# Kernel optimization log

Hardware: AMD Instinct MI355X
Metric: run time of the kernel (lower is better)

The kernel has to match this reference:

```python
import jax, jax.numpy as jnp
import numpy as np
from jax import lax

D_MODEL = 1024
D_INNER = 2048
B = 8
T = 2048
INIT_ALPHA_BIAS = 2.0


def setup_inputs() -> dict:
    key = jax.random.key(0)
    ks = jax.random.split(key, 6)
    def xavier(k, shape):
        fan_in, fan_out = shape[1], shape[0]
        lim = float(np.sqrt(6.0 / (fan_in + fan_out)))
        return jax.random.uniform(k, shape, jnp.float32, -lim, lim)
    return {
        "x": jax.random.normal(ks[0], (B, T, D_MODEL), jnp.float32),
        "h0": jnp.zeros((B, D_INNER), jnp.float32),
        "W_in": xavier(ks[1], (D_INNER, D_MODEL)),
        "W_alpha": xavier(ks[2], (D_INNER, D_INNER)),
        "b_alpha": jnp.full((D_INNER,), INIT_ALPHA_BIAS, jnp.float32),
        "W_v": xavier(ks[3], (D_INNER, D_INNER)),
        "b_v": jnp.zeros((D_INNER,), jnp.float32),
        "W_out": xavier(ks[4], (D_MODEL, D_INNER)),
    }


def reference(x, h0, W_in, W_alpha, b_alpha, W_v, b_v, W_out):
    # in_proj + silu pre-activation: [B,T,D_inner]
    x_proj = jax.nn.silu(jnp.einsum('btd,id->bti', x, W_in))
    # time-major for the scan: [T,B,D_inner]
    xr = jnp.transpose(x_proj, (1, 0, 2))
    # precompute gate and value for all steps (big GEMMs)
    alpha = jax.nn.sigmoid(jnp.einsum('tbd,ed->tbe', xr, W_alpha) + b_alpha)
    v = jnp.einsum('tbd,ed->tbe', xr, W_v) + b_v

    def step(h, av):
        a, vt = av
        h_new = a * h + (1.0 - a) * vt  # decay-gated update
        out_t = h_new * jax.nn.silu(h_new)  # self-gating
        return h_new, out_t

    h_final, outs = lax.scan(step, h0, (alpha, v))  # outs: [T,B,D_inner]
    # out_proj back to model dim, batch-major: [B,T,D_model]
    output = jnp.einsum('tbe,de->btd', outs, W_out)
    return output, h_final
```

## Files before the change

kernel.cpp:

```cpp
#include <hip/hip_runtime.h>
#include <cstdint>
#include <cstddef>

typedef unsigned short u16;
typedef unsigned int   u32;

#define D_MODEL 1024
#define D_INNER 2048
#define BATCH   8
#define TSEQ    2048
#define MROWS   (BATCH*TSEQ)
#define CHUNK   32
#define NCHUNK  (TSEQ/CHUNK)
#define EDIM    (BATCH*D_INNER)

typedef float  f32x4  __attribute__((ext_vector_type(4)));
typedef __bf16 bf16x8 __attribute__((ext_vector_type(8)));
typedef short  s16x8  __attribute__((ext_vector_type(8)));

__device__ __forceinline__ float bf2f(u16 u){ return __builtin_bit_cast(float, (u32)u << 16); }
__device__ __forceinline__ u16 f2bf(float f){
  u32 u = __builtin_bit_cast(u32, f);
  u += 0x7fffu + ((u >> 16) & 1u);
  return (u16)(u >> 16);
}
__device__ __forceinline__ float sigm(float x){ return 1.0f/(1.0f + __expf(-x)); }

__device__ __forceinline__ void gld16(const u16* g, u16* l){
  __builtin_amdgcn_global_load_lds((const __attribute__((address_space(1))) void*)g,
                                   (__attribute__((address_space(3))) void*)l, 16, 0, 0);
}

__device__ __forceinline__ s16x8 cvt8(const float* s){
  float4 u0 = *(const float4*)s;
  float4 u1 = *(const float4*)(s + 4);
  s16x8 p;
  p[0]=(short)f2bf(u0.x); p[1]=(short)f2bf(u0.y);
  p[2]=(short)f2bf(u0.z); p[3]=(short)f2bf(u0.w);
  p[4]=(short)f2bf(u1.x); p[5]=(short)f2bf(u1.y);
  p[6]=(short)f2bf(u1.z); p[7]=(short)f2bf(u1.w);
  return p;
}

#define LOADA(AF, MH) \
  _Pragma("unroll") \
  for (int mf = 0; mf < 4; ++mf){ \
    AF[mf][0] = *(const s16x8*)(As + (wr*128 + (MH)*64 + mf*16 + l15)*128 + csw); \
    AF[mf][1] = *(const s16x8*)(As + (wr*128 + (MH)*64 + mf*16 + l15)*128 + (csw^64)); \
  }
#define LOADB(BF, NH) \
  _Pragma("unroll") \
  for (int nf = 0; nf < 2; ++nf){ \
    BF[nf][0] = *(const s16x8*)(Bs + (wc*64 + (NH)*32 + nf*16 + l15)*128 + csw); \
    BF[nf][1] = *(const s16x8*)(Bs + (wc*64 + (NH)*32 + nf*16 + l15)*128 + (csw^64)); \
  }
#define MFMAQ(AF, BF, MH, NH) \
  __builtin_amdgcn_s_setprio(1); \
  _Pragma("unroll") \
  for (int mf = 0; mf < 4; ++mf) \
    _Pragma("unroll") \
    for (int nf = 0; nf < 2; ++nf) \
      _Pragma("unroll") \
      for (int ks = 0; ks < 2; ++ks) \
        acc[(MH)*4+mf][(NH)*2+nf] = __builtin_amdgcn_mfma_f32_16x16x32_bf16( \
            __builtin_bit_cast(bf16x8, AF[mf][ks]), \
            __builtin_bit_cast(bf16x8, BF[nf][ks]), \
            acc[(MH)*4+mf][(NH)*2+nf], 0, 0, 0); \
  __builtin_amdgcn_s_setprio(0);

template<int MODE, int K, int N>
__global__ __launch_bounds__(512, 2) void gemm256(
    const u16* __restrict__ A, const u16* __restrict__ Bt,
    const float* __restrict__ bias, const float* __restrict__ bias2,
    void* __restrict__ Cout, void* __restrict__ Cout2)
{
  __shared__ __align__(16) u16 sAB[2][2][16384];
  constexpr int NT = K/64;
  const int tid = threadIdx.x;
  const int w = tid >> 6, lane = tid & 63;
  const int wr = w >> 2, wc = w & 3;
  const int l15 = lane & 15, kg = lane >> 4;
  const int bm = blockIdx.x, bn = blockIdx.y;

  const int st_rw   = lane >> 3;
  const int st_cole = ((lane&7) ^ st_rw) << 3;
  const size_t a_base = (size_t)(bm*256)*K + st_cole;
  const size_t b_base = (size_t)(bn*256)*K + st_cole;

  auto stageA = [&](int buf, int kt, int set){
    u16* dst = &sAB[0][buf][set*4096 + w*512];
    #pragma unroll
    for (int i = 0; i < 2; ++i){
      const int row = set*64 + i*128 + w*8 + st_rw;
      gld16(A + a_base + (size_t)row*K + kt*64, dst + i*8192);
    }
  };
  auto stageB = [&](int buf, int kt, int set){
    #pragma unroll
    for (int i = 0; i < 2; ++i){
      const int g = i*64 + w*8;
      const int rowbase = (g>>5)*64 + set*32 + (g&31);
      gld16(Bt + b_base + (size_t)(rowbase + st_rw)*K + kt*64,
            &sAB[1][buf][rowbase*64]);
    }
  };

  const int csw = (kg*16) ^ ((l15&7)<<4);

  f32x4 acc[8][4] = {};

  stageB(0,0,0); stageA(0,0,0); stageB(0,0,1); stageA(0,0,1);
  asm volatile("s_waitcnt vmcnt(4)" ::: "memory");
  __builtin_amdgcn_s_barrier();

  for (int t = 0; t < NT; ++t){
    const char* As = (const char*)&sAB[0][t&1][0];
    const char* Bs = (const char*)&sAB[1][t&1][0];
    const int nb = (t+1)&1;
    const bool more = (t < NT-1);
    s16x8 af[4][2], bf0[2][2], bf1[2][2];

    LOADA(af, 0)
    LOADB(bf0, 0)
    if (more){
      stageB(nb, t+1, 0); stageA(nb, t+1, 0);
      asm volatile("s_waitcnt vmcnt(6)" ::: "memory");
    } else {
      asm volatile("s_waitcnt vmcnt(2)" ::: "memory");
    }
    __builtin_amdgcn_s_barrier();
    MFMAQ(af, bf0, 0, 0)
    __builtin_amdgcn_s_barrier();

    LOADB(bf1, 1)
    if (more){
      stageB(nb, t+1, 1);
      asm volatile("s_waitcnt vmcnt(6)" ::: "memory");
    } else {
      asm volatile("s_waitcnt vmcnt(0)" ::: "memory");
    }
    __builtin_amdgcn_s_barrier();
    MFMAQ(af, bf1, 0, 1)
    __builtin_amdgcn_s_barrier();

    LOADA(af, 1)
    if (more){ stageA(nb, t+1, 1); }
    __builtin_amdgcn_s_barrier();
    MFMAQ(af, bf1, 1, 1)
    __builtin_amdgcn_s_barrier();

    if (more){
      asm volatile("s_waitcnt vmcnt(4)" ::: "memory");
    }
    __builtin_amdgcn_s_barrier();
    MFMAQ(af, bf0, 1, 0)
    __builtin_amdgcn_s_barrier();
  }

  #pragma unroll
  for (int mi = 0; mi < 8; ++mi){
    #pragma unroll
    for (int ni = 0; ni < 4; ++ni){
      #pragma unroll
      for (int r = 0; r < 4; ++r){
        const int row = bm*256 + wr*128 + mi*16 + kg*4 + r;
        const int col = bn*256 + wc*64 + ni*16 + l15;
        float val = acc[mi][ni][r];
        if constexpr (MODE == 0){
          val = val * sigm(val);
          ((u16*)Cout)[(size_t)row*N + col] = f2bf(val);
        } else if constexpr (MODE == 3){
          const int orow = (row & 7)*TSEQ + (row >> 3);
          ((float*)Cout)[(size_t)orow*N + col] = val;
        } else if constexpr (MODE == 4){
          if (col < D_INNER){
            val = sigm(val + bias[col]);
            ((u16*)Cout)[(size_t)row*D_INNER + col] = f2bf(val);
          } else {
            val = val + bias2[col - D_INNER];
            ((u16*)Cout2)[(size_t)row*D_INNER + (col - D_INNER)] = f2bf(val);
          }
        }
      }
    }
  }
}

template<int MODE, int K, int N, bool BA, bool BB>
__global__ __launch_bounds__(256) void gemm_bt(
    const void* __restrict__ Ap, const void* __restrict__ Bp,
    const float* __restrict__ bias, void* __restrict__ Cout)
{
  __shared__ __align__(16) u16 sA[128*32];
  __shared__ __align__(16) u16 sB[128*32];
  const int tid = threadIdx.x;
  const int bm = blockIdx.x, bn = blockIdx.y;
  const int w = tid >> 6, lane = tid & 63;
  const int wr = w >> 1, wc = w & 1;
  const int l15 = lane & 15, kg = lane >> 4;
  const int r0   = tid >> 2;
  const int koff = (tid & 3) * 8;

  int ga[2];
  #pragma unroll
  for (int i = 0; i < 2; ++i){
    int mc = bm*128 + r0 + i*64;
    if (MODE == 0)      ga[i] = (mc & 7) * TSEQ + (mc >> 3);
    else if (MODE == 3) ga[i] = (mc & (TSEQ-1)) * BATCH + (mc >> 11);
    else                ga[i] = mc;
  }
  const u16*   Abf = (const u16*)Ap;
  const float* Af  = (const float*)Ap;
  const u16*   Bbf = (const u16*)Bp;
  const float* Bf  = (const float*)Bp;
  u16* la[2] = { sA + w*512, sA + 2048 + w*512 };
  u16* lb[2] = { sB + w*512, sB + 2048 + w*512 };
  u16* ldsA = sA + tid*8;
  u16* ldsB = sB + tid*8;
  const int gb[2] = { bn*128 + r0, bn*128 + r0 + 64 };

  f32x4 acc[4][4] = {};
  for (int kt = 0; kt < K/32; ++kt){
    __syncthreads();
    if constexpr (BA){
      gld16(Abf + (size_t)ga[0]*K + koff + kt*32, la[0]);
      gld16(Abf + (size_t)ga[1]*K + koff + kt*32, la[1]);
    } else {
      #pragma unroll
      for (int i = 0; i < 2; ++i)
        *(s16x8*)(ldsA + i*2048) = cvt8(Af + (size_t)ga[i]*K + koff + kt*32);
    }
    if constexpr (BB){
      gld16(Bbf + (size_t)gb[0]*K + koff + kt*32, lb[0]);
      gld16(Bbf + (size_t)gb[1]*K + koff + kt*32, lb[1]);
    } else {
      #pragma unroll
      for (int i = 0; i < 2; ++i)
        *(s16x8*)(ldsB + i*2048) = cvt8(Bf + (size_t)gb[i]*K + koff + kt*32);
    }
    __syncthreads();

    s16x8 af[4], bfr[4];
    #pragma unroll
    for (int m = 0; m < 4; ++m)
      af[m] = *(const s16x8*)(sA + (wr*64 + m*16 + l15)*32 + kg*8);
    #pragma unroll
    for (int n = 0; n < 4; ++n)
      bfr[n] = *(const s16x8*)(sB + (wc*64 + n*16 + l15)*32 + kg*8);
    #pragma unroll
    for (int m = 0; m < 4; ++m)
      #pragma unroll
      for (int n = 0; n < 4; ++n)
        acc[m][n] = __builtin_amdgcn_mfma_f32_16x16x32_bf16(
            __builtin_bit_cast(bf16x8, af[m]),
            __builtin_bit_cast(bf16x8, bfr[n]),
            acc[m][n], 0, 0, 0);
  }
  #pragma unroll
  for (int m = 0; m < 4; ++m)
    #pragma unroll
    for (int n = 0; n < 4; ++n)
      #pragma unroll
      for (int r = 0; r < 4; ++r){
        const int row = bm*128 + wr*64 + m*16 + kg*4 + r;
        const int col = bn*128 + wc*64 + n*16 + l15;
        float val = acc[m][n][r];
        if constexpr (MODE == 0){
          val = val * sigm(val);
          ((u16*)Cout)[(size_t)row*N + col] = f2bf(val);
        } else if constexpr (MODE == 1){
          val = sigm(val + bias[col]);
          ((u16*)Cout)[(size_t)row*N + col] = f2bf(val);
        } else if constexpr (MODE == 2){
          val = val + bias[col];
          ((u16*)Cout)[(size_t)row*N + col] = f2bf(val);
        } else {
          ((float*)Cout)[(size_t)row*N + col] = val;
        }
      }
}

__global__ __launch_bounds__(256) void scan_pass1(
    const u16* __restrict__ alpha, const u16* __restrict__ v,
    float* __restrict__ P, float* __restrict__ H)
{
  const int e = blockIdx.x*256 + threadIdx.x;
  const int c = blockIdx.y;
  const size_t base = (size_t)c*CHUNK*EDIM + e;
  float p = 1.f, h = 0.f;
  #pragma unroll 8
  for (int t = 0; t < CHUNK; ++t){
    float a  = bf2f(alpha[base + (size_t)t*EDIM]);
    float vv = bf2f(v[base + (size_t)t*EDIM]);
    p *= a;
    h = a*h + (1.f - a)*vv;
  }
  P[(size_t)c*EDIM + e] = p;
  H[(size_t)c*EDIM + e] = h;
}

__global__ __launch_bounds__(256) void scan_pass2(
    const float* __restrict__ P, const float* __restrict__ H,
    const float* __restrict__ h0, float* __restrict__ hstart,
    float* __restrict__ hfinal)
{
  const int e = blockIdx.x*256 + threadIdx.x;
  float hs = h0[e];
  for (int c = 0; c < NCHUNK; ++c){
    hstart[(size_t)c*EDIM + e] = hs;
    hs = P[(size_t)c*EDIM + e]*hs + H[(size_t)c*EDIM + e];
  }
  hfinal[e] = hs;
}

__global__ __launch_bounds__(256) void scan_pass3(
    const u16* __restrict__ alpha, const u16* __restrict__ v,
    const float* __restrict__ hstart, u16* __restrict__ outs)
{
  const int e = blockIdx.x*256 + threadIdx.x;
  const int c = blockIdx.y;
  const size_t base = (size_t)c*CHUNK*EDIM + e;
  float h = hstart[(size_t)c*EDIM + e];
  #pragma unroll 8
  for (int t = 0; t < CHUNK; ++t){
    float a  = bf2f(alpha[base + (size_t)t*EDIM]);
    float vv = bf2f(v[base + (size_t)t*EDIM]);
    h = a*h + (1.f - a)*vv;
    float o = h*h*sigm(h);
    outs[base + (size_t)t*EDIM] = f2bf(o);
  }
}

__global__ __launch_bounds__(256) void cvt_bf16(
    const float* __restrict__ src, u16* __restrict__ dst, int n4)
{
  const int i = blockIdx.x*256 + threadIdx.x;
  if (i >= n4) return;
  const float4 f = ((const float4*)src)[i];
  u32 w0 = (u32)f2bf(f.x) | ((u32)f2bf(f.y) << 16);
  u32 w1 = (u32)f2bf(f.z) | ((u32)f2bf(f.w) << 16);
  ((uint2*)dst)[i] = make_uint2(w0, w1);
}

__global__ __launch_bounds__(256) void cvt_x_tm(
    const float* __restrict__ src, u16* __restrict__ dst)
{
  const int i = blockIdx.x*256 + threadIdx.x;
  const int d4  = i & 255;
  const int rin = i >> 8;
  const int b = rin >> 11, tt = rin & (TSEQ-1);
  const int rout = tt*BATCH + b;
  const float4 f = ((const float4*)src)[i];
  u32 w0 = (u32)f2bf(f.x) | ((u32)f2bf(f.y) << 16);
  u32 w1 = (u32)f2bf(f.z) | ((u32)f2bf(f.w) << 16);
  ((uint2*)dst)[(size_t)rout*256 + d4] = make_uint2(w0, w1);
}

extern "C" void kernel_launch(void* const* d_in, const int* in_sizes, int n_in,
                              void* d_out, int out_size, void* d_ws, size_t ws_size,
                              hipStream_t stream)
{
  const float* x     = (const float*)d_in[0];
  const float* h0    = (const float*)d_in[1];
  const float* W_in  = (const float*)d_in[2];
  const float* W_al  = (const float*)d_in[3];
  const float* b_al  = (const float*)d_in[4];
  const float* W_v   = (const float*)d_in[5];
  const float* b_v   = (const float*)d_in[6];
  const float* W_out = (const float*)d_in[7];

  float* out  = (float*)d_out;
  float* hfin = out + (size_t)MROWS*D_MODEL;

  const size_t SZ_ACT = (size_t)MROWS*D_INNER*2;
  const size_t SZ_ST  = (size_t)NCHUNK*EDIM*4;
  const size_t SZ_WI  = (size_t)D_INNER*D_MODEL*2;
  const size_t SZ_WA  = (size_t)D_INNER*D_INNER*2;
  const size_t need_min  = 3*SZ_ACT + 3*SZ_ST;
  const size_t need_fast = need_min + 2*SZ_WI + 2*SZ_WA + 8192;

  if (ws_size < need_min) return;

  char* ws = (char*)d_ws;
  auto carve = [&](size_t bytes){
    char* p = ws; ws += (bytes + 255) & ~(size_t)255; return p;
  };
  u16* xp   = (u16*)carve(SZ_ACT);
  u16* alp  = (u16*)carve(SZ_ACT);
  u16* vv   = (u16*)carve(SZ_ACT);
  float* P  = (float*)carve(SZ_ST);
  float* H  = (float*)carve(SZ_ST);
  float* hs = (float*)carve(SZ_ST);

  const dim3 gScan(EDIM/256, NCHUNK);

  auto cvt = [&](const float* s, u16* d, size_t n){
    int n4 = (int)(n/4);
    cvt_bf16<<<(n4+255)/256, 256, 0, stream>>>(s, d, n4);
  };

  if (ws_size >= need_fast){
    u16* wib = (u16*)carve(SZ_WI);
    u16* wab = (u16*)carve(SZ_WA);
    u16* wvb = (u16*)carve(SZ_WA);
    u16* wob = (u16*)carve(SZ_WI);
    u16* xb  = alp;

    cvt_x_tm<<<(MROWS*D_MODEL/4)/256, 256, 0, stream>>>(x, xb);
    cvt(W_in,  wib, (size_t)D_INNER*D_MODEL);
    cvt(W_al,  wab, (size_t)D_INNER*D_INNER);
    cvt(W_v,   wvb, (size_t)D_INNER*D_INNER);
    cvt(W_out, wob, (size_t)D_MODEL*D_INNER);

    gemm256<0, D_MODEL, D_INNER><<<dim3(MROWS/256, D_INNER/256), 512, 0, stream>>>(
        xb, wib, nullptr, nullptr, xp, nullptr);
    gemm256<4, D_INNER, 2*D_INNER><<<dim3(MROWS/256, 2*D_INNER/256), 512, 0, stream>>>(
        xp, wab, b_al, b_v, alp, vv);

    scan_pass1<<<gScan, 256, 0, stream>>>(alp, vv, P, H);
    scan_pass2<<<EDIM/256, 256, 0, stream>>>(P, H, h0, hs, hfin);
    scan_pass3<<<gScan, 256, 0, stream>>>(alp, vv, hs, vv);

    gemm256<3, D_INNER, D_MODEL><<<dim3(MROWS/256, D_MODEL/256), 512, 0, stream>>>(
        vv, wob, nullptr, nullptr, out, nullptr);
  } else {
    const dim3 gBig(MROWS/128, D_INNER/128);
    const dim3 gOut(MROWS/128, D_MODEL/128);
    gemm_bt<0, D_MODEL, D_INNER, false, false><<<gBig, 256, 0, stream>>>(x,  W_in, nullptr, xp);
    gemm_bt<1, D_INNER, D_INNER, true,  false><<<gBig, 256, 0, stream>>>(xp, W_al, b_al,    alp);
    gemm_bt<2, D_INNER, D_INNER, true,  false><<<gBig, 256, 0, stream>>>(xp, W_v,  b_v,     vv);

    scan_pass1<<<gScan, 256, 0, stream>>>(alp, vv, P, H);
    scan_pass2<<<EDIM/256, 256, 0, stream>>>(P, H, h0, hs, hfin);
    scan_pass3<<<gScan, 256, 0, stream>>>(alp, vv, hs, vv);

    gemm_bt<3, D_INNER, D_MODEL, true, false><<<gOut, 256, 0, stream>>>(vv, W_out, nullptr, out);
  }
}
```

Baseline: 538.9 us.

## Simplify GEMM main loop to one barrier per K-tile with full prefetch

Replaces the four-phase interleaved GEMM schedule with a simpler one. Each K-tile now waits for all outstanding global-to-LDS loads and hits a single barrier. It then issues all next-tile loads at once and runs the full 8x4 MFMA block, loading all B fragments up front. This removes the many intermediate barriers, the partial vmcnt waits and the s_setprio hints, in exchange for coarser overlap and a full memory drain at each tile boundary, with more B fragments held in registers.

```diff
diff --git a/kernel.cpp b/kernel.cpp
--- a/kernel.cpp
+++ b/kernel.cpp
@@ -42,32 +42,6 @@
   return p;
 }
 
-#define LOADA(AF, MH) \
-  _Pragma("unroll") \
-  for (int mf = 0; mf < 4; ++mf){ \
-    AF[mf][0] = *(const s16x8*)(As + (wr*128 + (MH)*64 + mf*16 + l15)*128 + csw); \
-    AF[mf][1] = *(const s16x8*)(As + (wr*128 + (MH)*64 + mf*16 + l15)*128 + (csw^64)); \
-  }
-#define LOADB(BF, NH) \
-  _Pragma("unroll") \
-  for (int nf = 0; nf < 2; ++nf){ \
-    BF[nf][0] = *(const s16x8*)(Bs + (wc*64 + (NH)*32 + nf*16 + l15)*128 + csw); \
-    BF[nf][1] = *(const s16x8*)(Bs + (wc*64 + (NH)*32 + nf*16 + l15)*128 + (csw^64)); \
-  }
-#define MFMAQ(AF, BF, MH, NH) \
-  __builtin_amdgcn_s_setprio(1); \
-  _Pragma("unroll") \
-  for (int mf = 0; mf < 4; ++mf) \
-    _Pragma("unroll") \
-    for (int nf = 0; nf < 2; ++nf) \
-      _Pragma("unroll") \
-      for (int ks = 0; ks < 2; ++ks) \
-        acc[(MH)*4+mf][(NH)*2+nf] = __builtin_amdgcn_mfma_f32_16x16x32_bf16( \
-            __builtin_bit_cast(bf16x8, AF[mf][ks]), \
-            __builtin_bit_cast(bf16x8, BF[nf][ks]), \
-            acc[(MH)*4+mf][(NH)*2+nf], 0, 0, 0); \
-  __builtin_amdgcn_s_setprio(0);
-
 template<int MODE, int K, int N>
 __global__ __launch_bounds__(512, 2) void gemm256(
     const u16* __restrict__ A, const u16* __restrict__ Bt,
@@ -109,52 +83,45 @@
 
   f32x4 acc[8][4] = {};
 
-  stageB(0,0,0); stageA(0,0,0); stageB(0,0,1); stageA(0,0,1);
-  asm volatile("s_waitcnt vmcnt(4)" ::: "memory");
-  __builtin_amdgcn_s_barrier();
+  stageB(0,0,0); stageB(0,0,1); stageA(0,0,0); stageA(0,0,1);
 
   for (int t = 0; t < NT; ++t){
     const char* As = (const char*)&sAB[0][t&1][0];
     const char* Bs = (const char*)&sAB[1][t&1][0];
     const int nb = (t+1)&1;
-    const bool more = (t < NT-1);
-    s16x8 af[4][2], bf0[2][2], bf1[2][2];
-
-    LOADA(af, 0)
-    LOADB(bf0, 0)
-    if (more){
-      stageB(nb, t+1, 0); stageA(nb, t+1, 0);
-      asm volatile("s_waitcnt vmcnt(6)" ::: "memory");
-    } else {
-      asm volatile("s_waitcnt vmcnt(2)" ::: "memory");
-    }
+
+    asm volatile("s_waitcnt vmcnt(0)" ::: "memory");
     __builtin_amdgcn_s_barrier();
-    MFMAQ(af, bf0, 0, 0)
-    __builtin_amdgcn_s_barrier();
-
-    LOADB(bf1, 1)
-    if (more){
-      stageB(nb, t+1, 1);
-      asm volatile("s_waitcnt vmcnt(6)" ::: "memory");
-    } else {
-      asm volatile("s_waitcnt vmcnt(0)" ::: "memory");
-    }
-    __builtin_amdgcn_s_barrier();
-    MFMAQ(af, bf1, 0, 1)
-    __builtin_amdgcn_s_barrier();
-
-    LOADA(af, 1)
-    if (more){ stageA(nb, t+1, 1); }
-    __builtin_amdgcn_s_barrier();
-    MFMAQ(af, bf1, 1, 1)
-    __builtin_amdgcn_s_barrier();
-
-    if (more){
-      asm volatile("s_waitcnt vmcnt(4)" ::: "memory");
-    }
-    __builtin_amdgcn_s_barrier();
-    MFMAQ(af, bf0, 1, 0)
-    __builtin_amdgcn_s_barrier();
+
+    if (t < NT-1){
+      stageB(nb,t+1,0); stageB(nb,t+1,1); stageA(nb,t+1,0); stageA(nb,t+1,1);
+    }
+
+    s16x8 bf[4][2];
+    #pragma unroll
+    for (int ni = 0; ni < 4; ++ni){
+      bf[ni][0] = *(const s16x8*)(Bs + (wc*64 + ni*16 + l15)*128 + csw);
+      bf[ni][1] = *(const s16x8*)(Bs + (wc*64 + ni*16 + l15)*128 + (csw^64));
+    }
+    #pragma unroll
+    for (int mh = 0; mh < 2; ++mh){
+      s16x8 af[4][2];
+      #pragma unroll
+      for (int mf = 0; mf < 4; ++mf){
+        af[mf][0] = *(const s16x8*)(As + (wr*128 + mh*64 + mf*16 + l15)*128 + csw);
+        af[mf][1] = *(const s16x8*)(As + (wr*128 + mh*64 + mf*16 + l15)*128 + (csw^64));
+      }
+      #pragma unroll
+      for (int mf = 0; mf < 4; ++mf)
+        #pragma unroll
+        for (int ni = 0; ni < 4; ++ni)
+          #pragma unroll
+          for (int ks = 0; ks < 2; ++ks)
+            acc[mh*4+mf][ni] = __builtin_amdgcn_mfma_f32_16x16x32_bf16(
+                __builtin_bit_cast(bf16x8, af[mf][ks]),
+                __builtin_bit_cast(bf16x8, bf[ni][ks]),
+                acc[mh*4+mf][ni], 0, 0, 0);
+    }
   }
 
   #pragma unroll
```

Result: no change. 539.7 us (+0.1%).
